# Performance work log

Measured on AMD Instinct MI355X. Metric: run time of the kernel, lower is better.

Reference implementation:

```python
import jax, jax.numpy as jnp
import numpy as np
from jax import lax

# dims: B=batch, T=seq_len, D=inputSize, H=hiddenSize, L=num_layers, N=3 cell nodes
B, T, D, H, L = 128, 64, 256, 256, 2
WSCALE = 0.05  # scale on randn weight init for numerical health (math unchanged)


def setup_inputs() -> dict:
    key = jax.random.key(0)
    ks = jax.random.split(key, 8)
    return {
        "x": jax.random.normal(ks[0], (B, T, D), dtype=jnp.float32),
        "hidden": jax.random.normal(ks[1], (L, B, H), dtype=jnp.float32),
        # per-timestep cell parameters (the torch module instantiates one cell per timestep)
        "Win0": jax.random.normal(ks[2], (T, D, H), dtype=jnp.float32) * WSCALE,
        "Wh0": jax.random.normal(ks[3], (T, 3, H, H), dtype=jnp.float32) * WSCALE,
        "b0": jax.random.normal(ks[4], (T, 3, H), dtype=jnp.float32) * WSCALE,
        "Win1": jax.random.normal(ks[5], (T, H, H), dtype=jnp.float32) * WSCALE,
        "Wh1": jax.random.normal(ks[6], (T, 3, H, H), dtype=jnp.float32) * WSCALE,
        "b1": jax.random.normal(ks[7], (T, 3, H), dtype=jnp.float32) * WSCALE,
    }


def _cell(xt, h, Win, Wh, b):
    # cellList=[0,0,1,0,2]: activations [tanh, relu, sigmoid], connections [0, 0]
    n0 = jnp.tanh(xt @ Win + h @ Wh[0] + b[0])          # node 0
    n1 = jax.nn.relu(n0 @ Wh[1] + b[1]) + n0            # node 1 (+ node 0 via connection)
    n2 = jax.nn.sigmoid(n1 @ Wh[2] + b[2]) + n0         # node 2 (+ node 0 via connection)
    # unconnected nodes = {1, 2} -> mean over their values
    return 0.5 * (n1 + n2)


def _run_layer(xs_tbd, h0, Win, Wh, b):
    def step(h, inp):
        xt, Wi, Whh, bt = inp
        hn = _cell(xt, h, Wi, Whh, bt)
        return hn, hn
    h_last, outs = lax.scan(step, h0, (xs_tbd, Win, Wh, b))
    return outs, h_last  # outs: [T,B,H]


def reference(x, hidden, Win0, Wh0, b0, Win1, Wh1, b1):
    x_t = jnp.transpose(x, (1, 0, 2))                    # [T,B,D] (batch_first input)
    out0, h0f = _run_layer(x_t, hidden[0], Win0, Wh0, b0)
    out1, h1f = _run_layer(out0, hidden[1], Win1, Wh1, b1)
    output = jnp.transpose(out1, (1, 0, 2))              # [B,T,H], batch_first
    hidden_out = jnp.stack([h0f, h1f], axis=0)           # [L,B,H]
    return output, hidden_out
```

## Files before the change

kernel.cpp:

```cpp
#include <hip/hip_runtime.h>


typedef _Float16 f16;
typedef __attribute__((ext_vector_type(8))) _Float16 f16x8;
typedef __attribute__((ext_vector_type(4))) float f32x4;
typedef __attribute__((ext_vector_type(4))) float float4v;

#define Tt 64
#define FLAG_MAGIC 0x52570000

__device__ __forceinline__ void sb() { __builtin_amdgcn_sched_barrier(0); }

template <int N>
__device__ __forceinline__ void waitvm() {
  __builtin_amdgcn_s_waitcnt(0x0F70 | (N & 15) | ((N >> 4) << 14));
}
__device__ __forceinline__ void waitlgkm0() { __builtin_amdgcn_s_waitcnt(0xC07F); }

__device__ __forceinline__ void barx() {
  asm volatile("s_waitcnt lgkmcnt(0)\n\ts_barrier" ::: "memory");
}

__device__ __forceinline__ void dma16(const void* g, void* l) {
  __builtin_amdgcn_global_load_lds(
      (const __attribute__((address_space(1))) unsigned int*)g,
      (__attribute__((address_space(3))) unsigned int*)l, 16, 0, 0);
}

__device__ __forceinline__ float tanh_fast(float x) {
  float xc = fminf(fmaxf(x, -15.f), 15.f);
  float e = __expf(2.f * xc);
  return (e - 1.f) / (e + 1.f);
}
__device__ __forceinline__ float sigmoid_fast(float x) { return 1.f / (1.f + __expf(-x)); }

__global__ __launch_bounds__(256) void transpose_cvt_kernel(
    const float* __restrict__ Wh0, const float* __restrict__ Win1,
    const float* __restrict__ Wh1,
    f16* __restrict__ Wh0T, f16* __restrict__ Win1T, f16* __restrict__ Wh1T) {
  __shared__ float tile[256 * 33];
  const int bid = blockIdx.x;
  const int mat = bid >> 3, n0 = (bid & 7) << 5;
  const float* src; f16* dst;
  if (mat < 192)      { src = Wh0  + (size_t)mat * 65536;         dst = Wh0T  + (size_t)mat * 65536; }
  else if (mat < 256) { src = Win1 + (size_t)(mat - 192) * 65536; dst = Win1T + (size_t)(mat - 192) * 65536; }
  else                { src = Wh1  + (size_t)(mat - 256) * 65536; dst = Wh1T  + (size_t)(mat - 256) * 65536; }
  const int tid = threadIdx.x;
  const int c2 = tid & 15, kl = tid >> 4;
#pragma unroll
  for (int p = 0; p < 16; ++p) {
    const int k = kl + p * 16;
    float2 v = *(const float2*)(src + k * 256 + n0 + c2 * 2);
    tile[k * 33 + c2 * 2]     = v.x;
    tile[k * 33 + c2 * 2 + 1] = v.y;
  }
  __syncthreads();
  const int n = tid & 7, c = tid >> 3;
#pragma unroll
  for (int it = 0; it < 4; ++it) {
    const int nn = n + it * 8;
    f16x8 vv;
#pragma unroll
    for (int i = 0; i < 8; ++i) vv[i] = (f16)tile[(c * 8 + i) * 33 + nn];
    *(f16x8*)((char*)dst + (size_t)(n0 + nn) * 512 + c * 16) = vv;
  }
}

__global__ __launch_bounds__(512, 2) void xw_kernel(
    const float* __restrict__ x, const float* __restrict__ Win0,
    const float* __restrict__ b0, float* __restrict__ xw) {
  const int t = blockIdx.x >> 3, bb = blockIdx.x & 7;
  const int rb = bb << 4;
  const int tid = threadIdx.x, lane = tid & 63, w = tid >> 6;
  const int q = lane >> 4, mn = lane & 15;
  const int nc = w * 32 + mn, dr = q * 4;
  const float* wt = Win0 + (size_t)t * 65536;
  const float4v* xr = (const float4v*)(x + ((size_t)(rb + mn) * Tt + t) * 256);
  f32x4 acc[2] = {{0.f,0.f,0.f,0.f},{0.f,0.f,0.f,0.f}};
#pragma unroll
  for (int kt = 0; kt < 8; ++kt) {
    const int k0 = kt * 32 + q * 8;
    float4v x0 = xr[k0 / 4], x1 = xr[k0 / 4 + 1];
    f16x8 a = {(f16)x0.x, (f16)x0.y, (f16)x0.z, (f16)x0.w,
               (f16)x1.x, (f16)x1.y, (f16)x1.z, (f16)x1.w};
#pragma unroll
    for (int nt = 0; nt < 2; ++nt) {
      f16x8 b;
#pragma unroll
      for (int j = 0; j < 8; ++j) b[j] = (f16)wt[(size_t)(k0 + j) * 256 + nc + nt * 16];
      acc[nt] = __builtin_amdgcn_mfma_f32_16x16x32_f16(a, b, acc[nt], 0, 0, 0);
    }
  }
#pragma unroll
  for (int nt = 0; nt < 2; ++nt) {
    const float bv = b0[(size_t)t * 768 + nc + nt * 16];
#pragma unroll
    for (int r = 0; r < 4; ++r)
      xw[(size_t)t * 32768 + (size_t)(rb + dr + r) * 256 + nc + nt * 16] = acc[nt][r] + bv;
  }
}

template <int NW, bool DMA>
__device__ __forceinline__ void phase(f32x4 (&acc)[2], const char* arow, const char* wb,
                                      const int (&bo)[4], const char* gnext, char* lnext,
                                      const int (&off)[8], int q) {
  waitvm<NW>();
  sb();
  f16x8 a[4], b[8];
#pragma unroll
  for (int kt = 0; kt < 4; ++kt) {
    a[kt]         = *(const f16x8*)(arow + kt * 64 + q * 16);
    b[kt * 2]     = *(const f16x8*)(wb + bo[kt]);
    b[kt * 2 + 1] = *(const f16x8*)(wb + bo[kt] + 4096);
  }
  sb();
  waitlgkm0();
  if (DMA) {
#pragma unroll
    for (int d = 0; d < 8; ++d) dma16(gnext + off[d], lnext + d * 1024);
  }
  sb();
#pragma unroll
  for (int kt = 0; kt < 4; ++kt) {
    acc[0] = __builtin_amdgcn_mfma_f32_16x16x32_f16(a[kt], b[kt * 2],     acc[0], 0, 0, 0);
    acc[1] = __builtin_amdgcn_mfma_f32_16x16x32_f16(a[kt], b[kt * 2 + 1], acc[1], 0, 0, 0);
  }
}

template <int NW>
__device__ __forceinline__ void phaseRA(f32x4 (&acc)[2], const f16x8* af, const char* wb,
                                        const int (&bo)[4], const char* gnext, char* lnext,
                                        const int (&off)[8]) {
  waitvm<NW>();
  sb();
  f16x8 b[8];
#pragma unroll
  for (int kt = 0; kt < 4; ++kt) {
    b[kt * 2]     = *(const f16x8*)(wb + bo[kt]);
    b[kt * 2 + 1] = *(const f16x8*)(wb + bo[kt] + 4096);
  }
  sb();
  waitlgkm0();
#pragma unroll
  for (int d = 0; d < 8; ++d) dma16(gnext + off[d], lnext + d * 1024);
  sb();
#pragma unroll
  for (int kt = 0; kt < 4; ++kt) {
    acc[0] = __builtin_amdgcn_mfma_f32_16x16x32_f16(af[kt], b[kt * 2],     acc[0], 0, 0, 0);
    acc[1] = __builtin_amdgcn_mfma_f32_16x16x32_f16(af[kt], b[kt * 2 + 1], acc[1], 0, 0, 0);
  }
}

__global__ __launch_bounds__(512, 1) void rnn_kernel(
    const float* __restrict__ hidden,
    const f16* __restrict__ Wh0T, const float* __restrict__ b0,
    const f16* __restrict__ Win1T, const f16* __restrict__ Wh1T, const float* __restrict__ b1,
    const float* __restrict__ xw, f16* __restrict__ hseq, int* __restrict__ flags,
    float* __restrict__ out) {
  __shared__ __align__(16) char smem[147968];
  char* wlds = smem;
  char* abuf = smem + 131072;
  char* nbuf = smem + 139520;

  const int tid = threadIdx.x;
  const int lane = tid & 63;
  const int w = tid >> 6;
  const int q = lane >> 4;
  const int mn = lane & 15;
  const bool isL0 = blockIdx.x < 8;
  const int g = blockIdx.x & 7;
  const int rb = g << 4;
  const int nc = w * 32 + mn;
  const int dr = q * 4;
  const int wslice = w * 16384;

  int off[8], bo[4];
#pragma unroll
  for (int d = 0; d < 8; ++d) {
    const int row = 4 * d + q;
    off[d] = row * 512 + ((mn ^ (row & 15)) << 4);
  }
#pragma unroll
  for (int kt = 0; kt < 4; ++kt)
    bo[kt] = mn * 256 + (((kt * 4 + q) ^ mn) << 4);

  const float* hsrc = hidden + (isL0 ? 0 : 32768) + (size_t)rb * 256;
  for (int i = tid; i < 16 * 256; i += 512) {
    const int m = i >> 8, n = i & 255;
    *(f16*)(abuf + m * 528 + n * 2) = (f16)hsrc[m * 256 + n];
  }

  char* bufA = wlds + wslice;
  char* bufB = bufA + 8192;
  const f32x4 zero4 = {0.f, 0.f, 0.f, 0.f};
  float n0v[2][4], n1v[2][4];

  if (isL0) {
    const char* WB = (const char*)Wh0T;
    {
      const char* gw = WB + wslice;
#pragma unroll
      for (int d = 0; d < 8; ++d) dma16(gw + off[d], bufA + d * 1024);
#pragma unroll
      for (int d = 0; d < 8; ++d) dma16(gw + 256 + off[d], bufB + d * 1024);
      sb();
    }
    barx();

#pragma unroll 1
    for (int t = 0; t < Tt; ++t) {
      const int tn = (t < Tt - 1) ? t + 1 : t;
      const bool last = (t == Tt - 1);
      const char* wt  = WB + (size_t)t * 393216 + wslice;
      const char* wtn = WB + (size_t)tn * 393216 + wslice;

      float xwv[2][4];
#pragma unroll
      for (int nt = 0; nt < 2; ++nt)
#pragma unroll
        for (int r = 0; r < 4; ++r)
          xwv[nt][r] = xw[(size_t)t * 32768 + (size_t)(rb + dr + r) * 256 + nc + nt * 16];
      const float bv1a = b0[(size_t)t * 768 + 256 + nc], bv1b = b0[(size_t)t * 768 + 256 + nc + 16];
      const float bv2a = b0[(size_t)t * 768 + 512 + nc], bv2b = b0[(size_t)t * 768 + 512 + nc + 16];
      sb();

      f32x4 acc[2];
      acc[0] = zero4; acc[1] = zero4;
      phase<20, true>(acc, abuf + mn * 528,       bufA, bo, wt + 131072,       bufA, off, q);
      phase<20, true>(acc, abuf + mn * 528 + 256, bufB, bo, wt + 131072 + 256, bufB, off, q);
      waitvm<20>();
      sb();
#pragma unroll
      for (int nt = 0; nt < 2; ++nt)
#pragma unroll
        for (int r = 0; r < 4; ++r) {
          float v = tanh_fast(acc[nt][r] + xwv[nt][r]);
          n0v[nt][r] = v;
          *(f16*)(nbuf + (dr + r) * 528 + (nc + nt * 16) * 2) = (f16)v;
        }
      barx();

      acc[0] = zero4; acc[1] = zero4;
      phase<8, true>(acc, nbuf + mn * 528,       bufA, bo, wt + 262144,       bufA, off, q);
      phase<8, true>(acc, nbuf + mn * 528 + 256, bufB, bo, wt + 262144 + 256, bufB, off, q);
      barx();
#pragma unroll
      for (int nt = 0; nt < 2; ++nt) {
        const float bv = nt ? bv1b : bv1a;
#pragma unroll
        for (int r = 0; r < 4; ++r) {
          float v = fmaxf(acc[nt][r] + bv, 0.f) + n0v[nt][r];
          n1v[nt][r] = v;
          *(f16*)(nbuf + (dr + r) * 528 + (nc + nt * 16) * 2) = (f16)v;
        }
      }
      barx();

      acc[0] = zero4; acc[1] = zero4;
      phase<8, false>(acc, nbuf + mn * 528,       bufA, bo, wt, bufA, off, q);
      phase<0, false>(acc, nbuf + mn * 528 + 256, bufB, bo, wt, bufB, off, q);
#pragma unroll
      for (int nt = 0; nt < 2; ++nt) {
        const float bv = nt ? bv2b : bv2a;
#pragma unroll
        for (int r = 0; r < 4; ++r) {
          float s = sigmoid_fast(acc[nt][r] + bv);
          float hv = 0.5f * (n1v[nt][r] + s + n0v[nt][r]);
          f16 h16 = (f16)hv;
          *(f16*)(abuf + (dr + r) * 528 + (nc + nt * 16) * 2) = h16;
          hseq[((size_t)(g * 64 + t)) * 4096 + (dr + r) * 256 + nc + nt * 16] = h16;
          if (last) out[2097152 + (size_t)(rb + dr + r) * 256 + nc + nt * 16] = hv;
        }
      }
      waitvm<0>();
      __threadfence();
      __syncthreads();
      if (tid == 0) {
        __hip_atomic_store(&flags[g * 64 + t], FLAG_MAGIC | (t + 1),
                           __ATOMIC_RELEASE, __HIP_MEMORY_SCOPE_AGENT);
      }
      sb();
      {
        const char* gw = wtn;
#pragma unroll
        for (int d = 0; d < 8; ++d) dma16(gw + off[d], bufA + d * 1024);
#pragma unroll
        for (int d = 0; d < 8; ++d) dma16(gw + 256 + off[d], bufB + d * 1024);
        sb();
      }
    }
  } else {
    const char* WI = (const char*)Win1T;
    const char* WH = (const char*)Wh1T;
    const f16* hsg = hseq + (size_t)g * 64 * 4096;
    {
      const char* gw = WH + wslice;
#pragma unroll
      for (int d = 0; d < 8; ++d) dma16(gw + off[d], bufA + d * 1024);
#pragma unroll
      for (int d = 0; d < 8; ++d) dma16(gw + 256 + off[d], bufB + d * 1024);
      sb();
    }
    barx();

#pragma unroll 1
    for (int t = 0; t < Tt; ++t) {
      const int tn = (t < Tt - 1) ? t + 1 : t;
      const bool last = (t == Tt - 1);
      const char* wit = WI + (size_t)t * 131072 + wslice;
      const char* wht = WH + (size_t)t * 393216 + wslice;
      const char* whn = WH + (size_t)tn * 393216 + wslice;

      {
        const int want = FLAG_MAGIC | (t + 1);
        while (__hip_atomic_load(&flags[g * 64 + t], __ATOMIC_ACQUIRE,
                                 __HIP_MEMORY_SCOPE_AGENT) != want) {}
      }
      sb();
      const char* ht = (const char*)(hsg + (size_t)t * 4096);
      f16x8 af[8];
#pragma unroll
      for (int kt = 0; kt < 8; ++kt)
        af[kt] = *(const f16x8*)(ht + mn * 512 + kt * 64 + q * 16);
      const float bv0a = b1[(size_t)t * 768 + nc],       bv0b = b1[(size_t)t * 768 + nc + 16];
      const float bv1a = b1[(size_t)t * 768 + 256 + nc], bv1b = b1[(size_t)t * 768 + 256 + nc + 16];
      const float bv2a = b1[(size_t)t * 768 + 512 + nc], bv2b = b1[(size_t)t * 768 + 512 + nc + 16];
      sb();

      f32x4 acc[2];
      acc[0] = zero4; acc[1] = zero4;
      phase<63, true>(acc, abuf + mn * 528,       bufA, bo, wit,       bufA, off, q);
      phase<63, true>(acc, abuf + mn * 528 + 256, bufB, bo, wit + 256, bufB, off, q);
      phaseRA<8>(acc, af,     bufA, bo, wht + 131072,       bufA, off);
      phaseRA<8>(acc, af + 4, bufB, bo, wht + 131072 + 256, bufB, off);
#pragma unroll
      for (int nt = 0; nt < 2; ++nt) {
        const float bv = nt ? bv0b : bv0a;
#pragma unroll
        for (int r = 0; r < 4; ++r) {
          float v = tanh_fast(acc[nt][r] + bv);
          n0v[nt][r] = v;
          *(f16*)(nbuf + (dr + r) * 528 + (nc + nt * 16) * 2) = (f16)v;
        }
      }
      barx();

      acc[0] = zero4; acc[1] = zero4;
      phase<8, true>(acc, nbuf + mn * 528,       bufA, bo, wht + 262144,       bufA, off, q);
      phase<8, true>(acc, nbuf + mn * 528 + 256, bufB, bo, wht + 262144 + 256, bufB, off, q);
      barx();
#pragma unroll
      for (int nt = 0; nt < 2; ++nt) {
        const float bv = nt ? bv1b : bv1a;
#pragma unroll
        for (int r = 0; r < 4; ++r) {
          float v = fmaxf(acc[nt][r] + bv, 0.f) + n0v[nt][r];
          n1v[nt][r] = v;
          *(f16*)(nbuf + (dr + r) * 528 + (nc + nt * 16) * 2) = (f16)v;
        }
      }
      barx();

      acc[0] = zero4; acc[1] = zero4;
      phase<8, true>(acc, nbuf + mn * 528,       bufA, bo, whn,       bufA, off, q);
      phase<8, true>(acc, nbuf + mn * 528 + 256, bufB, bo, whn + 256, bufB, off, q);
#pragma unroll
      for (int nt = 0; nt < 2; ++nt) {
        const float bv = nt ? bv2b : bv2a;
#pragma unroll
        for (int r = 0; r < 4; ++r) {
          float s = sigmoid_fast(acc[nt][r] + bv);
          float hv = 0.5f * (n1v[nt][r] + s + n0v[nt][r]);
          *(f16*)(abuf + (dr + r) * 528 + (nc + nt * 16) * 2) = (f16)hv;
          out[((size_t)(rb + dr + r) * Tt + t) * 256 + nc + nt * 16] = hv;
          if (last) out[2097152 + 32768 + (size_t)(rb + dr + r) * 256 + nc + nt * 16] = hv;
        }
      }
      barx();
    }
  }
}

extern "C" void kernel_launch(void* const* d_in, const int* in_sizes, int n_in,
                              void* d_out, int out_size, void* d_ws, size_t ws_size,
                              hipStream_t stream) {
  (void)in_sizes; (void)n_in; (void)out_size; (void)ws_size;
  const float* x      = (const float*)d_in[0];
  const float* hidden = (const float*)d_in[1];
  const float* Win0   = (const float*)d_in[2];
  const float* Wh0    = (const float*)d_in[3];
  const float* b0     = (const float*)d_in[4];
  const float* Win1   = (const float*)d_in[5];
  const float* Wh1    = (const float*)d_in[6];
  const float* b1     = (const float*)d_in[7];
  float* out = (float*)d_out;

  char* ws = (char*)d_ws;
  f16* Wh0T  = (f16*)(ws);
  f16* Win1T = (f16*)(ws + 25165824);
  f16* Wh1T  = (f16*)(ws + 33554432);
  float* xw  = (float*)(ws + 58720256);
  f16* hseq  = (f16*)(ws + 67108864);
  int* flags = (int*)(ws + 71303168);

  transpose_cvt_kernel<<<dim3(3584), dim3(256), 0, stream>>>(
      Wh0, Win1, Wh1, Wh0T, Win1T, Wh1T);
  xw_kernel<<<dim3(512), dim3(512), 0, stream>>>(x, Win0, b0, xw);
  rnn_kernel<<<dim3(16), dim3(512), 0, stream>>>(
      hidden, Wh0T, b0, Win1T, Wh1T, b1, xw, hseq, flags, out);
}
```

Measured before the change: 796.1 us.

## Split each RNN row group across two blocks by hidden half with flag sync

The recurrent kernel now runs 32 blocks instead of 16, with each batch row group split across two blocks that each own half of the hidden columns. Intermediate node activations and hidden states are exchanged through global scratch buffers with per-node release/acquire flags, and each block computes its local-half partial product before waiting on the peer half. Win0 is also pre-transposed to fp16 so the xw kernel loads vectorized weights instead of strided scalar floats. This doubles the compute units used on the serial chain and halves the per-block weight streaming, at the cost of extra cross-block flag round trips on every node of every timestep.

Measured after the change: 2.106 ms. +164.5%, slower.

```diff
diff --git a/kernel.cpp b/kernel.cpp
--- a/kernel.cpp
+++ b/kernel.cpp
@@ -9,6 +9,16 @@
 #define Tt 64
 #define FLAG_MAGIC 0x52570000
 
+#define WS_WH0T   0
+#define WS_WIN1T  25165824
+#define WS_WH1T   33554432
+#define WS_WIN0T  58720256
+#define WS_XW     67108864
+#define WS_HSEQ   75497472
+#define WS_NX     79691776
+#define WS_H1X    96468992
+#define WS_FLAGS  100663296
+
 __device__ __forceinline__ void sb() { __builtin_amdgcn_sched_barrier(0); }
 
 template <int N>
@@ -34,17 +44,71 @@
 }
 __device__ __forceinline__ float sigmoid_fast(float x) { return 1.f / (1.f + __expf(-x)); }
 
+__device__ __forceinline__ void dmaHalf(const char* gsrc, char* ldst, const int (&off)[4]) {
+#pragma unroll
+  for (int d = 0; d < 4; ++d) dma16(gsrc + off[d], ldst + d * 1024);
+}
+__device__ __forceinline__ void loadB(f16x8 (&b)[4], const char* wb, const int (&bo)[4]) {
+#pragma unroll
+  for (int kt = 0; kt < 4; ++kt) b[kt] = *(const f16x8*)(wb + bo[kt]);
+}
+__device__ __forceinline__ void loadA_lds(f16x8 (&a)[4], const char* aP, int q) {
+#pragma unroll
+  for (int kt = 0; kt < 4; ++kt) a[kt] = *(const f16x8*)(aP + kt * 64 + q * 16);
+}
+__device__ __forceinline__ void loadA_g(f16x8 (&a)[4], const char* gp, int stride, int q, int mn) {
+#pragma unroll
+  for (int kt = 0; kt < 4; ++kt)
+    a[kt] = *(const f16x8*)(gp + mn * stride + kt * 64 + q * 16);
+}
+__device__ __forceinline__ void loadA_f32(f16x8 (&a)[4], const float* hp, int colbase, int q, int mn) {
+#pragma unroll
+  for (int kt = 0; kt < 4; ++kt) {
+    const float4v* p = (const float4v*)(hp + mn * 256 + colbase + kt * 32 + q * 8);
+    float4v x0 = p[0], x1 = p[1];
+    f16x8 v;
+    v[0] = (f16)x0.x; v[1] = (f16)x0.y; v[2] = (f16)x0.z; v[3] = (f16)x0.w;
+    v[4] = (f16)x1.x; v[5] = (f16)x1.y; v[6] = (f16)x1.z; v[7] = (f16)x1.w;
+    a[kt] = v;
+  }
+}
+__device__ __forceinline__ void mfma4(f32x4& acc, const f16x8 (&a)[4], const f16x8 (&b)[4]) {
+#pragma unroll
+  for (int kt = 0; kt < 4; ++kt)
+    acc = __builtin_amdgcn_mfma_f32_16x16x32_f16(a[kt], b[kt], acc, 0, 0, 0);
+}
+
+__device__ __forceinline__ size_t nx_off(int l, int g, int t, int node, int nh) {
+  return (size_t)((((l * 8 + g) * 64 + t) * 2 + node) * 2 + nh) * 4096;
+}
+__device__ __forceinline__ int fnidx(int l, int g, int t, int node, int nh) {
+  return 1024 + ((((l * 8 + g) * 64 + t) * 2 + node) * 2 + nh);
+}
+
+__device__ __forceinline__ void publish(int* f, int tag) {
+  waitvm<0>();
+  __threadfence();
+  __syncthreads();
+  if (threadIdx.x == 0)
+    __hip_atomic_store(f, tag, __ATOMIC_RELEASE, __HIP_MEMORY_SCOPE_AGENT);
+}
+__device__ __forceinline__ void acquire(const int* f, int tag) {
+  while (__hip_atomic_load(f, __ATOMIC_ACQUIRE, __HIP_MEMORY_SCOPE_AGENT) != tag) {}
+}
+
 __global__ __launch_bounds__(256) void transpose_cvt_kernel(
     const float* __restrict__ Wh0, const float* __restrict__ Win1,
-    const float* __restrict__ Wh1,
-    f16* __restrict__ Wh0T, f16* __restrict__ Win1T, f16* __restrict__ Wh1T) {
+    const float* __restrict__ Wh1, const float* __restrict__ Win0,
+    f16* __restrict__ Wh0T, f16* __restrict__ Win1T, f16* __restrict__ Wh1T,
+    f16* __restrict__ Win0T) {
   __shared__ float tile[256 * 33];
   const int bid = blockIdx.x;
   const int mat = bid >> 3, n0 = (bid & 7) << 5;
   const float* src; f16* dst;
   if (mat < 192)      { src = Wh0  + (size_t)mat * 65536;         dst = Wh0T  + (size_t)mat * 65536; }
   else if (mat < 256) { src = Win1 + (size_t)(mat - 192) * 65536; dst = Win1T + (size_t)(mat - 192) * 65536; }
-  else                { src = Wh1  + (size_t)(mat - 256) * 65536; dst = Wh1T  + (size_t)(mat - 256) * 65536; }
+  else if (mat < 448) { src = Wh1  + (size_t)(mat - 256) * 65536; dst = Wh1T  + (size_t)(mat - 256) * 65536; }
+  else                { src = Win0 + (size_t)(mat - 448) * 65536; dst = Win0T + (size_t)(mat - 448) * 65536; }
   const int tid = threadIdx.x;
   const int c2 = tid & 15, kl = tid >> 4;
 #pragma unroll
@@ -67,14 +131,13 @@
 }
 
 __global__ __launch_bounds__(512, 2) void xw_kernel(
-    const float* __restrict__ x, const float* __restrict__ Win0,
+    const float* __restrict__ x, const f16* __restrict__ Win0T,
     const float* __restrict__ b0, float* __restrict__ xw) {
   const int t = blockIdx.x >> 3, bb = blockIdx.x & 7;
   const int rb = bb << 4;
   const int tid = threadIdx.x, lane = tid & 63, w = tid >> 6;
-  const int q = lane >> 4, mn = lane & 15;
-  const int nc = w * 32 + mn, dr = q * 4;
-  const float* wt = Win0 + (size_t)t * 65536;
+  const int q = lane >> 4, mn = lane & 15, dr = q * 4;
+  const f16* wt = Win0T + (size_t)t * 65536;
   const float4v* xr = (const float4v*)(x + ((size_t)(rb + mn) * Tt + t) * 256);
   f32x4 acc[2] = {{0.f,0.f,0.f,0.f},{0.f,0.f,0.f,0.f}};
 #pragma unroll
@@ -85,298 +148,306 @@
                (f16)x1.x, (f16)x1.y, (f16)x1.z, (f16)x1.w};
 #pragma unroll
     for (int nt = 0; nt < 2; ++nt) {
-      f16x8 b;
-#pragma unroll
-      for (int j = 0; j < 8; ++j) b[j] = (f16)wt[(size_t)(k0 + j) * 256 + nc + nt * 16];
+      f16x8 b = *(const f16x8*)(wt + (size_t)(w * 32 + nt * 16 + mn) * 256 + k0);
       acc[nt] = __builtin_amdgcn_mfma_f32_16x16x32_f16(a, b, acc[nt], 0, 0, 0);
     }
   }
 #pragma unroll
   for (int nt = 0; nt < 2; ++nt) {
-    const float bv = b0[(size_t)t * 768 + nc + nt * 16];
+    const int n = w * 32 + nt * 16 + mn;
+    const float bv = b0[(size_t)t * 768 + n];
 #pragma unroll
     for (int r = 0; r < 4; ++r)
-      xw[(size_t)t * 32768 + (size_t)(rb + dr + r) * 256 + nc + nt * 16] = acc[nt][r] + bv;
-  }
-}
-
-template <int NW, bool DMA>
-__device__ __forceinline__ void phase(f32x4 (&acc)[2], const char* arow, const char* wb,
-                                      const int (&bo)[4], const char* gnext, char* lnext,
-                                      const int (&off)[8], int q) {
-  waitvm<NW>();
-  sb();
-  f16x8 a[4], b[8];
-#pragma unroll
-  for (int kt = 0; kt < 4; ++kt) {
-    a[kt]         = *(const f16x8*)(arow + kt * 64 + q * 16);
-    b[kt * 2]     = *(const f16x8*)(wb + bo[kt]);
-    b[kt * 2 + 1] = *(const f16x8*)(wb + bo[kt] + 4096);
-  }
-  sb();
-  waitlgkm0();
-  if (DMA) {
-#pragma unroll
-    for (int d = 0; d < 8; ++d) dma16(gnext + off[d], lnext + d * 1024);
-  }
-  sb();
-#pragma unroll
-  for (int kt = 0; kt < 4; ++kt) {
-    acc[0] = __builtin_amdgcn_mfma_f32_16x16x32_f16(a[kt], b[kt * 2],     acc[0], 0, 0, 0);
-    acc[1] = __builtin_amdgcn_mfma_f32_16x16x32_f16(a[kt], b[kt * 2 + 1], acc[1], 0, 0, 0);
-  }
-}
-
-template <int NW>
-__device__ __forceinline__ void phaseRA(f32x4 (&acc)[2], const f16x8* af, const char* wb,
-                                        const int (&bo)[4], const char* gnext, char* lnext,
-                                        const int (&off)[8]) {
-  waitvm<NW>();
-  sb();
-  f16x8 b[8];
-#pragma unroll
-  for (int kt = 0; kt < 4; ++kt) {
-    b[kt * 2]     = *(const f16x8*)(wb + bo[kt]);
-    b[kt * 2 + 1] = *(const f16x8*)(wb + bo[kt] + 4096);
-  }
-  sb();
-  waitlgkm0();
-#pragma unroll
-  for (int d = 0; d < 8; ++d) dma16(gnext + off[d], lnext + d * 1024);
-  sb();
-#pragma unroll
-  for (int kt = 0; kt < 4; ++kt) {
-    acc[0] = __builtin_amdgcn_mfma_f32_16x16x32_f16(af[kt], b[kt * 2],     acc[0], 0, 0, 0);
-    acc[1] = __builtin_amdgcn_mfma_f32_16x16x32_f16(af[kt], b[kt * 2 + 1], acc[1], 0, 0, 0);
+      xw[(size_t)t * 32768 + (size_t)(rb + dr + r) * 256 + n] = acc[nt][r] + bv;
   }
 }
 
 __global__ __launch_bounds__(512, 1) void rnn_kernel(
     const float* __restrict__ hidden,
     const f16* __restrict__ Wh0T, const float* __restrict__ b0,
-    const f16* __restrict__ Win1T, const f16* __restrict__ Wh1T, const float* __restrict__ b1,
-    const float* __restrict__ xw, f16* __restrict__ hseq, int* __restrict__ flags,
-    float* __restrict__ out) {
-  __shared__ __align__(16) char smem[147968];
+    const f16* __restrict__ Win1T, const f16* __restrict__ Wh1T,
+    const float* __restrict__ b1, const float* __restrict__ xw,
+    char* __restrict__ hseqb, char* __restrict__ nxb, char* __restrict__ h1xb,
+    int* __restrict__ flags, float* __restrict__ out) {
+  __shared__ __align__(16) char smem[98304];
   char* wlds = smem;
-  char* abuf = smem + 131072;
-  char* nbuf = smem + 139520;
+  char* abuf = smem + 65536;
+  char* nbuf = smem + 69888;
 
   const int tid = threadIdx.x;
-  const int lane = tid & 63;
-  const int w = tid >> 6;
-  const int q = lane >> 4;
-  const int mn = lane & 15;
-  const bool isL0 = blockIdx.x < 8;
-  const int g = blockIdx.x & 7;
-  const int rb = g << 4;
-  const int nc = w * 32 + mn;
-  const int dr = q * 4;
-  const int wslice = w * 16384;
-
-  int off[8], bo[4];
-#pragma unroll
-  for (int d = 0; d < 8; ++d) {
+  const int lane = tid & 63, w = tid >> 6;
+  const int q = lane >> 4, mn = lane & 15;
+  const bool isL0 = blockIdx.x < 16;
+  const int g = (blockIdx.x >> 1) & 7;
+  const int nh = blockIdx.x & 1, ph = nh ^ 1;
+  const int rb = g << 4, dr = q * 4;
+  const int nc = nh * 128 + w * 16 + mn;
+  const int wwb = nh * 65536 + w * 8192;
+
+  char* bufA = wlds + w * 8192;
+  char* bufB = bufA + 4096;
+
+  int off[4], bo[4];
+#pragma unroll
+  for (int d = 0; d < 4; ++d) {
     const int row = 4 * d + q;
-    off[d] = row * 512 + ((mn ^ (row & 15)) << 4);
+    off[d] = row * 512 + ((mn ^ row) << 4);
   }
 #pragma unroll
   for (int kt = 0; kt < 4; ++kt)
     bo[kt] = mn * 256 + (((kt * 4 + q) ^ mn) << 4);
 
   const float* hsrc = hidden + (isL0 ? 0 : 32768) + (size_t)rb * 256;
-  for (int i = tid; i < 16 * 256; i += 512) {
-    const int m = i >> 8, n = i & 255;
-    *(f16*)(abuf + m * 528 + n * 2) = (f16)hsrc[m * 256 + n];
-  }
-
-  char* bufA = wlds + wslice;
-  char* bufB = bufA + 8192;
+  for (int i = tid; i < 2048; i += 512) {
+    const int m = i >> 7, kl = i & 127;
+    *(f16*)(abuf + m * 272 + kl * 2) = (f16)hsrc[m * 256 + nh * 128 + kl];
+  }
+
   const f32x4 zero4 = {0.f, 0.f, 0.f, 0.f};
-  float n0v[2][4], n1v[2][4];
 
   if (isL0) {
     const char* WB = (const char*)Wh0T;
-    {
-      const char* gw = WB + wslice;
-#pragma unroll
-      for (int d = 0; d < 8; ++d) dma16(gw + off[d], bufA + d * 1024);
-#pragma unroll
-      for (int d = 0; d < 8; ++d) dma16(gw + 256 + off[d], bufB + d * 1024);
-      sb();
-    }
+    { const char* w0 = WB + wwb;
+      dmaHalf(w0 + nh * 256, bufA, off);
+      dmaHalf(w0 + ph * 256, bufB, off); }
     barx();
 
 #pragma unroll 1
     for (int t = 0; t < Tt; ++t) {
-      const int tn = (t < Tt - 1) ? t + 1 : t;
       const bool last = (t == Tt - 1);
-      const char* wt  = WB + (size_t)t * 393216 + wslice;
-      const char* wtn = WB + (size_t)tn * 393216 + wslice;
-
-      float xwv[2][4];
-#pragma unroll
-      for (int nt = 0; nt < 2; ++nt)
+      const char* wt = WB + (size_t)t * 393216 + wwb;
+      const int tag = FLAG_MAGIC | (t + 1);
+
+      f16x8 a[4], b[4], af[4];
+      f32x4 acc = zero4;
+      waitvm<4>(); sb();
+      loadA_lds(a, abuf + mn * 272, q);
+      loadB(b, bufA, bo);
+      waitlgkm0(); sb();
+      mfma4(acc, a, b);
+      sb();
+      if (t > 0) acquire(&flags[(g * 64 + t - 1) * 2 + ph], FLAG_MAGIC | t);
+      sb();
+      float xwv[4];
+#pragma unroll
+      for (int r = 0; r < 4; ++r)
+        xwv[r] = xw[(size_t)t * 32768 + (size_t)(rb + dr + r) * 256 + nc];
+      const float bv1 = b0[(size_t)t * 768 + 256 + nc];
+      const float bv2 = b0[(size_t)t * 768 + 512 + nc];
+      if (t > 0) loadA_g(af, hseqb + (size_t)(g * 64 + t - 1) * 8192 + ph * 256, 512, q, mn);
+      else       loadA_f32(af, hsrc, ph * 128, q, mn);
+      dmaHalf(wt + 131072 + nh * 256, bufA, off);
+      sb();
+      waitvm<18>(); sb();
+      loadB(b, bufB, bo);
+      waitlgkm0(); sb();
+      mfma4(acc, af, b);
+      sb();
+      float n0v[4];
+#pragma unroll
+      for (int r = 0; r < 4; ++r) {
+        float v = tanh_fast(acc[r] + xwv[r]);
+        n0v[r] = v;
+        *(f16*)(nbuf + (dr + r) * 272 + (w * 16 + mn) * 2) = (f16)v;
+      }
+      { char* slot = nxb + nx_off(0, g, t, 0, nh);
 #pragma unroll
         for (int r = 0; r < 4; ++r)
-          xwv[nt][r] = xw[(size_t)t * 32768 + (size_t)(rb + dr + r) * 256 + nc + nt * 16];
-      const float bv1a = b0[(size_t)t * 768 + 256 + nc], bv1b = b0[(size_t)t * 768 + 256 + nc + 16];
-      const float bv2a = b0[(size_t)t * 768 + 512 + nc], bv2b = b0[(size_t)t * 768 + 512 + nc + 16];
-      sb();
-
-      f32x4 acc[2];
-      acc[0] = zero4; acc[1] = zero4;
-      phase<20, true>(acc, abuf + mn * 528,       bufA, bo, wt + 131072,       bufA, off, q);
-      phase<20, true>(acc, abuf + mn * 528 + 256, bufB, bo, wt + 131072 + 256, bufB, off, q);
-      waitvm<20>();
-      sb();
-#pragma unroll
-      for (int nt = 0; nt < 2; ++nt)
-#pragma unroll
-        for (int r = 0; r < 4; ++r) {
-          float v = tanh_fast(acc[nt][r] + xwv[nt][r]);
-          n0v[nt][r] = v;
-          *(f16*)(nbuf + (dr + r) * 528 + (nc + nt * 16) * 2) = (f16)v;
-        }
+          *(f16*)(slot + (dr + r) * 256 + (w * 16 + mn) * 2) = (f16)n0v[r]; }
+      publish(&flags[fnidx(0, g, t, 0, nh)], tag);
+      acc = zero4;
+      loadA_lds(a, nbuf + mn * 272, q);
+      loadB(b, bufA, bo);
+      waitlgkm0(); sb();
+      dmaHalf(wt + 131072 + ph * 256, bufB, off);
+      sb();
+      mfma4(acc, a, b);
+      sb();
+      acquire(&flags[fnidx(0, g, t, 0, ph)], tag);
+      sb();
+      loadA_g(af, nxb + nx_off(0, g, t, 0, ph), 256, q, mn);
+      dmaHalf(wt + 262144 + nh * 256, bufA, off);
+      sb();
+      loadB(b, bufB, bo);
+      waitlgkm0(); sb();
+      mfma4(acc, af, b);
+      sb();
+      float n1v[4];
+#pragma unroll
+      for (int r = 0; r < 4; ++r) n1v[r] = fmaxf(acc[r] + bv1, 0.f) + n0v[r];
       barx();
-
-      acc[0] = zero4; acc[1] = zero4;
-      phase<8, true>(acc, nbuf + mn * 528,       bufA, bo, wt + 262144,       bufA, off, q);
-      phase<8, true>(acc, nbuf + mn * 528 + 256, bufB, bo, wt + 262144 + 256, bufB, off, q);
-      barx();
-#pragma unroll
-      for (int nt = 0; nt < 2; ++nt) {
-        const float bv = nt ? bv1b : bv1a;
-#pragma unroll
-        for (int r = 0; r < 4; ++r) {
-          float v = fmaxf(acc[nt][r] + bv, 0.f) + n0v[nt][r];
-          n1v[nt][r] = v;
-          *(f16*)(nbuf + (dr + r) * 528 + (nc + nt * 16) * 2) = (f16)v;
-        }
-      }
-      barx();
-
-      acc[0] = zero4; acc[1] = zero4;
-      phase<8, false>(acc, nbuf + mn * 528,       bufA, bo, wt, bufA, off, q);
-      phase<0, false>(acc, nbuf + mn * 528 + 256, bufB, bo, wt, bufB, off, q);
-#pragma unroll
-      for (int nt = 0; nt < 2; ++nt) {
-        const float bv = nt ? bv2b : bv2a;
-#pragma unroll
-        for (int r = 0; r < 4; ++r) {
-          float s = sigmoid_fast(acc[nt][r] + bv);
-          float hv = 0.5f * (n1v[nt][r] + s + n0v[nt][r]);
-          f16 h16 = (f16)hv;
-          *(f16*)(abuf + (dr + r) * 528 + (nc + nt * 16) * 2) = h16;
-          hseq[((size_t)(g * 64 + t)) * 4096 + (dr + r) * 256 + nc + nt * 16] = h16;
-          if (last) out[2097152 + (size_t)(rb + dr + r) * 256 + nc + nt * 16] = hv;
-        }
-      }
-      waitvm<0>();
-      __threadfence();
-      __syncthreads();
-      if (tid == 0) {
-        __hip_atomic_store(&flags[g * 64 + t], FLAG_MAGIC | (t + 1),
-                           __ATOMIC_RELEASE, __HIP_MEMORY_SCOPE_AGENT);
-      }
-      sb();
-      {
-        const char* gw = wtn;
-#pragma unroll
-        for (int d = 0; d < 8; ++d) dma16(gw + off[d], bufA + d * 1024);
-#pragma unroll
-        for (int d = 0; d < 8; ++d) dma16(gw + 256 + off[d], bufB + d * 1024);
-        sb();
+#pragma unroll
+      for (int r = 0; r < 4; ++r)
+        *(f16*)(nbuf + (dr + r) * 272 + (w * 16 + mn) * 2) = (f16)n1v[r];
+      { char* slot = nxb + nx_off(0, g, t, 1, nh);
+#pragma unroll
+        for (int r = 0; r < 4; ++r)
+          *(f16*)(slot + (dr + r) * 256 + (w * 16 + mn) * 2) = (f16)n1v[r]; }
+      publish(&flags[fnidx(0, g, t, 1, nh)], tag);
+      acc = zero4;
+      loadA_lds(a, nbuf + mn * 272, q);
+      loadB(b, bufA, bo);
+      waitlgkm0(); sb();
+      dmaHalf(wt + 262144 + ph * 256, bufB, off);
+      sb();
+      mfma4(acc, a, b);
+      sb();
+      acquire(&flags[fnidx(0, g, t, 1, ph)], tag);
+      sb();
+      loadA_g(af, nxb + nx_off(0, g, t, 1, ph), 256, q, mn);
+      sb();
+      loadB(b, bufB, bo);
+      waitlgkm0(); sb();
+      mfma4(acc, af, b);
+      sb();
+#pragma unroll
+      for (int r = 0; r < 4; ++r) {
+        float s = sigmoid_fast(acc[r] + bv2);
+        float hv = 0.5f * (n1v[r] + s + n0v[r]);
+        f16 h16 = (f16)hv;
+        *(f16*)(abuf + (dr + r) * 272 + (w * 16 + mn) * 2) = h16;
+        *(f16*)(hseqb + (size_t)(g * 64 + t) * 8192 + (dr + r) * 512 + nc * 2) = h16;
+        if (last) out[2097152 + (size_t)(rb + dr + r) * 256 + nc] = hv;
+      }
+      publish(&flags[(g * 64 + t) * 2 + nh], tag);
+      if (!last) {
+        const char* wn = WB + (size_t)(t + 1) * 393216 + wwb;
+        dmaHalf(wn + nh * 256, bufA, off);
+        dmaHalf(wn + ph * 256, bufB, off);
       }
     }
   } else {
     const char* WI = (const char*)Win1T;
     const char* WH = (const char*)Wh1T;
-    const f16* hsg = hseq + (size_t)g * 64 * 4096;
-    {
-      const char* gw = WH + wslice;
-#pragma unroll
-      for (int d = 0; d < 8; ++d) dma16(gw + off[d], bufA + d * 1024);
-#pragma unroll
-      for (int d = 0; d < 8; ++d) dma16(gw + 256 + off[d], bufB + d * 1024);
-      sb();
-    }
+    { const char* w0 = WH + wwb;
+      dmaHalf(w0 + nh * 256, bufA, off);
+      dmaHalf(w0 + ph * 256, bufB, off); }
     barx();
 
 #pragma unroll 1
     for (int t = 0; t < Tt; ++t) {
-      const int tn = (t < Tt - 1) ? t + 1 : t;
       const bool last = (t == Tt - 1);
-      const char* wit = WI + (size_t)t * 131072 + wslice;
-      const char* wht = WH + (size_t)t * 393216 + wslice;
-      const char* whn = WH + (size_t)tn * 393216 + wslice;
-
-      {
-        const int want = FLAG_MAGIC | (t + 1);
-        while (__hip_atomic_load(&flags[g * 64 + t], __ATOMIC_ACQUIRE,
-                                 __HIP_MEMORY_SCOPE_AGENT) != want) {}
-      }
-      sb();
-      const char* ht = (const char*)(hsg + (size_t)t * 4096);
-      f16x8 af[8];
-#pragma unroll
-      for (int kt = 0; kt < 8; ++kt)
-        af[kt] = *(const f16x8*)(ht + mn * 512 + kt * 64 + q * 16);
-      const float bv0a = b1[(size_t)t * 768 + nc],       bv0b = b1[(size_t)t * 768 + nc + 16];
-      const float bv1a = b1[(size_t)t * 768 + 256 + nc], bv1b = b1[(size_t)t * 768 + 256 + nc + 16];
-      const float bv2a = b1[(size_t)t * 768 + 512 + nc], bv2b = b1[(size_t)t * 768 + 512 + nc + 16];
-      sb();
-
-      f32x4 acc[2];
-      acc[0] = zero4; acc[1] = zero4;
-      phase<63, true>(acc, abuf + mn * 528,       bufA, bo, wit,       bufA, off, q);
-      phase<63, true>(acc, abuf + mn * 528 + 256, bufB, bo, wit + 256, bufB, off, q);
-      phaseRA<8>(acc, af,     bufA, bo, wht + 131072,       bufA, off);
-      phaseRA<8>(acc, af + 4, bufB, bo, wht + 131072 + 256, bufB, off);
-#pragma unroll
-      for (int nt = 0; nt < 2; ++nt) {
-        const float bv = nt ? bv0b : bv0a;
-#pragma unroll
-        for (int r = 0; r < 4; ++r) {
-          float v = tanh_fast(acc[nt][r] + bv);
-          n0v[nt][r] = v;
-          *(f16*)(nbuf + (dr + r) * 528 + (nc + nt * 16) * 2) = (f16)v;
-        }
-      }
+      const char* wht = WH + (size_t)t * 393216 + wwb;
+      const char* wit = WI + (size_t)t * 131072 + wwb;
+      const int tag = FLAG_MAGIC | (t + 1);
+
+      f16x8 a[4], b[4], af[4], ah[4];
+      f32x4 acc = zero4;
+      waitvm<4>(); sb();
+      loadA_lds(a, abuf + mn * 272, q);
+      loadB(b, bufA, bo);
+      waitlgkm0(); sb();
+      mfma4(acc, a, b);
+      sb();
+      if (t > 0) acquire(&flags[5120 + (g * 64 + t - 1) * 2 + ph], FLAG_MAGIC | t);
+      sb();
+      const float bv0 = b1[(size_t)t * 768 + nc];
+      const float bv1 = b1[(size_t)t * 768 + 256 + nc];
+      const float bv2 = b1[(size_t)t * 768 + 512 + nc];
+      if (t > 0) loadA_g(af, h1xb + (size_t)((g * 64 + t - 1) * 2 + ph) * 4096, 256, q, mn);
+      else       loadA_f32(af, hsrc, ph * 128, q, mn);
+      dmaHalf(wit + 0, bufA, off);
+      sb();
+      waitvm<15>(); sb();
+      loadB(b, bufB, bo);
+      waitlgkm0(); sb();
+      mfma4(acc, af, b);
+      sb();
+      { const unsigned long long want2 =
+            ((unsigned long long)(unsigned)tag << 32) | (unsigned)tag;
+        const unsigned long long* fp = (const unsigned long long*)&flags[(g * 64 + t) * 2];
+        while (__hip_atomic_load(fp, __ATOMIC_ACQUIRE, __HIP_MEMORY_SCOPE_AGENT) != want2) {} }
+      sb();
+      dmaHalf(wit + 256, bufB, off);
+      loadA_g(af, hseqb + (size_t)(g * 64 + t) * 8192, 512, q, mn);
+      loadA_g(ah, hseqb + (size_t)(g * 64 + t) * 8192 + 256, 512, q, mn);
+      sb();
+      loadB(b, bufA, bo);
+      waitlgkm0(); sb();
+      dmaHalf(wht + 131072 + nh * 256, bufA, off);
+      sb();
+      mfma4(acc, af, b);
+      sb();
+      waitvm<12>(); sb();
+      loadB(b, bufB, bo);
+      waitlgkm0(); sb();
+      dmaHalf(wht + 131072 + ph * 256, bufB, off);
+      sb();
+      mfma4(acc, ah, b);
+      sb();
+      float n0v[4];
+#pragma unroll
+      for (int r = 0; r < 4; ++r) {
+        float v = tanh_fast(acc[r] + bv0);
+        n0v[r] = v;
+        *(f16*)(nbuf + (dr + r) * 272 + (w * 16 + mn) * 2) = (f16)v;
+      }
+      { char* slot = nxb + nx_off(1, g, t, 0, nh);
+#pragma unroll
+        for (int r = 0; r < 4; ++r)
+          *(f16*)(slot + (dr + r) * 256 + (w * 16 + mn) * 2) = (f16)n0v[r]; }
+      publish(&flags[fnidx(1, g, t, 0, nh)], tag);
+      acc = zero4;
+      loadA_lds(a, nbuf + mn * 272, q);
+      loadB(b, bufA, bo);
+      waitlgkm0(); sb();
+      dmaHalf(wht + 262144 + nh * 256, bufA, off);
+      sb();
+      mfma4(acc, a, b);
+      sb();
+      acquire(&flags[fnidx(1, g, t, 0, ph)], tag);
+      sb();
+      loadA_g(af, nxb + nx_off(1, g, t, 0, ph), 256, q, mn);
+      sb();
+      loadB(b, bufB, bo);
+      waitlgkm0(); sb();
+      dmaHalf(wht + 262144 + ph * 256, bufB, off);
+      sb();
+      mfma4(acc, af, b);
+      sb();
+      float n1v[4];
+#pragma unroll
+      for (int r = 0; r < 4; ++r) n1v[r] = fmaxf(acc[r] + bv1, 0.f) + n0v[r];
       barx();
-
-      acc[0] = zero4; acc[1] = zero4;
-      phase<8, true>(acc, nbuf + mn * 528,       bufA, bo, wht + 262144,       bufA, off, q);
-      phase<8, true>(acc, nbuf + mn * 528 + 256, bufB, bo, wht + 262144 + 256, bufB, off, q);
-      barx();
-#pragma unroll
-      for (int nt = 0; nt < 2; ++nt) {
-        const float bv = nt ? bv1b : bv1a;
-#pragma unroll
-        for (int r = 0; r < 4; ++r) {
-          float v = fmaxf(acc[nt][r] + bv, 0.f) + n0v[nt][r];
-          n1v[nt][r] = v;
-          *(f16*)(nbuf + (dr + r) * 528 + (nc + nt * 16) * 2) = (f16)v;
-        }
-      }
-      barx();
-
-      acc[0] = zero4; acc[1] = zero4;
-      phase<8, true>(acc, nbuf + mn * 528,       bufA, bo, whn,       bufA, off, q);
-      phase<8, true>(acc, nbuf + mn * 528 + 256, bufB, bo, whn + 256, bufB, off, q);
-#pragma unroll
-      for (int nt = 0; nt < 2; ++nt) {
-        const float bv = nt ? bv2b : bv2a;
-#pragma unroll
-        for (int r = 0; r < 4; ++r) {
-          float s = sigmoid_fast(acc[nt][r] + bv);
-          float hv = 0.5f * (n1v[nt][r] + s + n0v[nt][r]);
-          *(f16*)(abuf + (dr + r) * 528 + (nc + nt * 16) * 2) = (f16)hv;
-          out[((size_t)(rb + dr + r) * Tt + t) * 256 + nc + nt * 16] = hv;
-          if (last) out[2097152 + 32768 + (size_t)(rb + dr + r) * 256 + nc + nt * 16] = hv;
-        }
-      }
-      barx();
+#pragma unroll
+      for (int r = 0; r < 4; ++r)
+        *(f16*)(nbuf + (dr + r) * 272 + (w * 16 + mn) * 2) = (f16)n1v[r];
+      { char* slot = nxb + nx_off(1, g, t, 1, nh);
+#pragma unroll
+        for (int r = 0; r < 4; ++r)
+          *(f16*)(slot + (dr + r) * 256 + (w * 16 + mn) * 2) = (f16)n1v[r]; }
+      publish(&flags[fnidx(1, g, t, 1, nh)], tag);
+      acc = zero4;
+      loadA_lds(a, nbuf + mn * 272, q);
+      loadB(b, bufA, bo);
+      waitlgkm0(); sb();
+      mfma4(acc, a, b);
+      sb();
+      acquire(&flags[fnidx(1, g, t, 1, ph)], tag);
+      sb();
+      loadA_g(af, nxb + nx_off(1, g, t, 1, ph), 256, q, mn);
+      sb();
+      loadB(b, bufB, bo);
+      waitlgkm0(); sb();
+      mfma4(acc, af, b);
+      sb();
+#pragma unroll
+      for (int r = 0; r < 4; ++r) {
+        float s = sigmoid_fast(acc[r] + bv2);
+        float hv = 0.5f * (n1v[r] + s + n0v[r]);
+        f16 h16 = (f16)hv;
+        *(f16*)(abuf + (dr + r) * 272 + (w * 16 + mn) * 2) = h16;
+        *(f16*)(h1xb + (size_t)((g * 64 + t) * 2 + nh) * 4096 +
+                (dr + r) * 256 + (w * 16 + mn) * 2) = h16;
+        out[((size_t)(rb + dr + r) * Tt + t) * 256 + nc] = hv;
+        if (last) out[2097152 + 32768 + (size_t)(rb + dr + r) * 256 + nc] = hv;
+      }
+      publish(&flags[5120 + (g * 64 + t) * 2 + nh], tag);
+      if (!last) {
+        const char* wn = WH + (size_t)(t + 1) * 393216 + wwb;
+        dmaHalf(wn + nh * 256, bufA, off);
+        dmaHalf(wn + ph * 256, bufB, off);
+      }
     }
   }
 }
@@ -396,16 +467,19 @@
   float* out = (float*)d_out;
 
   char* ws = (char*)d_ws;
-  f16* Wh0T  = (f16*)(ws);
-  f16* Win1T = (f16*)(ws + 25165824);
-  f16* Wh1T  = (f16*)(ws + 33554432);
-  float* xw  = (float*)(ws + 58720256);
-  f16* hseq  = (f16*)(ws + 67108864);
-  int* flags = (int*)(ws + 71303168);
-
-  transpose_cvt_kernel<<<dim3(3584), dim3(256), 0, stream>>>(
-      Wh0, Win1, Wh1, Wh0T, Win1T, Wh1T);
-  xw_kernel<<<dim3(512), dim3(512), 0, stream>>>(x, Win0, b0, xw);
-  rnn_kernel<<<dim3(16), dim3(512), 0, stream>>>(
-      hidden, Wh0T, b0, Win1T, Wh1T, b1, xw, hseq, flags, out);
-}
+  f16* Wh0T  = (f16*)(ws + WS_WH0T);
+  f16* Win1T = (f16*)(ws + WS_WIN1T);
+  f16* Wh1T  = (f16*)(ws + WS_WH1T);
+  f16* Win0T = (f16*)(ws + WS_WIN0T);
+  float* xwp = (float*)(ws + WS_XW);
+  char* hseq = ws + WS_HSEQ;
+  char* nx   = ws + WS_NX;
+  char* h1x  = ws + WS_H1X;
+  int* flags = (int*)(ws + WS_FLAGS);
+
+  transpose_cvt_kernel<<<dim3(4096), dim3(256), 0, stream>>>(
+      Wh0, Win1, Wh1, Win0, Wh0T, Win1T, Wh1T, Win0T);
+  xw_kernel<<<dim3(512), dim3(512), 0, stream>>>(x, Win0T, b0, xwp);
+  rnn_kernel<<<dim3(32), dim3(512), 0, stream>>>(
+      hidden, Wh0T, b0, Win1T, Wh1T, b1, xwp, hseq, nx, h1x, flags, out);
+}
```

## Pre-transpose Win0 to fp16 and place RNN blocks on chosen XCDs

Applied to the files above, without the earlier changes.

Win0 is now converted to transposed fp16 in the existing transpose kernel, so xw_kernel can load its B operands as one 16-byte vector instead of eight strided fp32 scalar loads. The rnn_kernel launches 32 blocks and keeps only the 16 that land on XCDs 0-1 (layer 0) and 4-5 (layer 1). This keeps each layer's blocks together so their cross-block flag and hidden-state traffic stays within a shared L2. The cost is an extra 16 MB transpose pass, more workspace, and reliance on round-robin block-to-XCD dispatch.

Measured after the change: 854.7 us. 1.07x slower.

```diff
diff --git a/kernel.cpp b/kernel.cpp
--- a/kernel.cpp
+++ b/kernel.cpp
@@ -9,6 +9,14 @@
 #define Tt 64
 #define FLAG_MAGIC 0x52570000
 
+#define WS_WH0T   0
+#define WS_WIN1T  25165824
+#define WS_WH1T   33554432
+#define WS_WIN0T  58720256
+#define WS_XW     67108864
+#define WS_HSEQ   75497472
+#define WS_FLAGS  79691776
+
 __device__ __forceinline__ void sb() { __builtin_amdgcn_sched_barrier(0); }
 
 template <int N>
@@ -36,15 +44,17 @@
 
 __global__ __launch_bounds__(256) void transpose_cvt_kernel(
     const float* __restrict__ Wh0, const float* __restrict__ Win1,
-    const float* __restrict__ Wh1,
-    f16* __restrict__ Wh0T, f16* __restrict__ Win1T, f16* __restrict__ Wh1T) {
+    const float* __restrict__ Wh1, const float* __restrict__ Win0,
+    f16* __restrict__ Wh0T, f16* __restrict__ Win1T, f16* __restrict__ Wh1T,
+    f16* __restrict__ Win0T) {
   __shared__ float tile[256 * 33];
   const int bid = blockIdx.x;
   const int mat = bid >> 3, n0 = (bid & 7) << 5;
   const float* src; f16* dst;
   if (mat < 192)      { src = Wh0  + (size_t)mat * 65536;         dst = Wh0T  + (size_t)mat * 65536; }
   else if (mat < 256) { src = Win1 + (size_t)(mat - 192) * 65536; dst = Win1T + (size_t)(mat - 192) * 65536; }
-  else                { src = Wh1  + (size_t)(mat - 256) * 65536; dst = Wh1T  + (size_t)(mat - 256) * 65536; }
+  else if (mat < 448) { src = Wh1  + (size_t)(mat - 256) * 65536; dst = Wh1T  + (size_t)(mat - 256) * 65536; }
+  else                { src = Win0 + (size_t)(mat - 448) * 65536; dst = Win0T + (size_t)(mat - 448) * 65536; }
   const int tid = threadIdx.x;
   const int c2 = tid & 15, kl = tid >> 4;
 #pragma unroll
@@ -67,14 +77,13 @@
 }
 
 __global__ __launch_bounds__(512, 2) void xw_kernel(
-    const float* __restrict__ x, const float* __restrict__ Win0,
+    const float* __restrict__ x, const f16* __restrict__ Win0T,
     const float* __restrict__ b0, float* __restrict__ xw) {
   const int t = blockIdx.x >> 3, bb = blockIdx.x & 7;
   const int rb = bb << 4;
   const int tid = threadIdx.x, lane = tid & 63, w = tid >> 6;
-  const int q = lane >> 4, mn = lane & 15;
-  const int nc = w * 32 + mn, dr = q * 4;
-  const float* wt = Win0 + (size_t)t * 65536;
+  const int q = lane >> 4, mn = lane & 15, dr = q * 4;
+  const f16* wt = Win0T + (size_t)t * 65536;
   const float4v* xr = (const float4v*)(x + ((size_t)(rb + mn) * Tt + t) * 256);
   f32x4 acc[2] = {{0.f,0.f,0.f,0.f},{0.f,0.f,0.f,0.f}};
 #pragma unroll
@@ -85,18 +94,17 @@
                (f16)x1.x, (f16)x1.y, (f16)x1.z, (f16)x1.w};
 #pragma unroll
     for (int nt = 0; nt < 2; ++nt) {
-      f16x8 b;
-#pragma unroll
-      for (int j = 0; j < 8; ++j) b[j] = (f16)wt[(size_t)(k0 + j) * 256 + nc + nt * 16];
+      f16x8 b = *(const f16x8*)(wt + (size_t)(w * 32 + nt * 16 + mn) * 256 + k0);
       acc[nt] = __builtin_amdgcn_mfma_f32_16x16x32_f16(a, b, acc[nt], 0, 0, 0);
     }
   }
 #pragma unroll
   for (int nt = 0; nt < 2; ++nt) {
-    const float bv = b0[(size_t)t * 768 + nc + nt * 16];
+    const int n = w * 32 + nt * 16 + mn;
+    const float bv = b0[(size_t)t * 768 + n];
 #pragma unroll
     for (int r = 0; r < 4; ++r)
-      xw[(size_t)t * 32768 + (size_t)(rb + dr + r) * 256 + nc + nt * 16] = acc[nt][r] + bv;
+      xw[(size_t)t * 32768 + (size_t)(rb + dr + r) * 256 + n] = acc[nt][r] + bv;
   }
 }
 
@@ -162,13 +170,17 @@
   char* abuf = smem + 131072;
   char* nbuf = smem + 139520;
 
+  const int xcd = blockIdx.x & 7, slot = blockIdx.x >> 3;
+  bool isL0; int g;
+  if (xcd < 2)                  { isL0 = true;  g = xcd * 4 + slot; }
+  else if (xcd >= 4 && xcd < 6) { isL0 = false; g = (xcd - 4) * 4 + slot; }
+  else return;
+
   const int tid = threadIdx.x;
   const int lane = tid & 63;
   const int w = tid >> 6;
   const int q = lane >> 4;
   const int mn = lane & 15;
-  const bool isL0 = blockIdx.x < 8;
-  const int g = blockIdx.x & 7;
   const int rb = g << 4;
   const int nc = w * 32 + mn;
   const int dr = q * 4;
@@ -396,16 +408,17 @@
   float* out = (float*)d_out;
 
   char* ws = (char*)d_ws;
-  f16* Wh0T  = (f16*)(ws);
-  f16* Win1T = (f16*)(ws + 25165824);
-  f16* Wh1T  = (f16*)(ws + 33554432);
-  float* xw  = (float*)(ws + 58720256);
-  f16* hseq  = (f16*)(ws + 67108864);
-  int* flags = (int*)(ws + 71303168);
-
-  transpose_cvt_kernel<<<dim3(3584), dim3(256), 0, stream>>>(
-      Wh0, Win1, Wh1, Wh0T, Win1T, Wh1T);
-  xw_kernel<<<dim3(512), dim3(512), 0, stream>>>(x, Win0, b0, xw);
-  rnn_kernel<<<dim3(16), dim3(512), 0, stream>>>(
-      hidden, Wh0T, b0, Win1T, Wh1T, b1, xw, hseq, flags, out);
-}
+  f16* Wh0T  = (f16*)(ws + WS_WH0T);
+  f16* Win1T = (f16*)(ws + WS_WIN1T);
+  f16* Wh1T  = (f16*)(ws + WS_WH1T);
+  f16* Win0T = (f16*)(ws + WS_WIN0T);
+  float* xwp = (float*)(ws + WS_XW);
+  f16* hseq  = (f16*)(ws + WS_HSEQ);
+  int* flags = (int*)(ws + WS_FLAGS);
+
+  transpose_cvt_kernel<<<dim3(4096), dim3(256), 0, stream>>>(
+      Wh0, Win1, Wh1, Win0, Wh0T, Win1T, Wh1T, Win0T);
+  xw_kernel<<<dim3(512), dim3(512), 0, stream>>>(x, Win0T, b0, xwp);
+  rnn_kernel<<<dim3(32), dim3(512), 0, stream>>>(
+      hidden, Wh0T, b0, Win1T, Wh1T, b1, xwp, hseq, flags, out);
+}
```
